# Kernel optimization log

Hardware: AMD Instinct MI355X
Metric: run time of the kernel (lower is better)

The kernel has to match this reference:

```python
import jax, jax.numpy as jnp
import numpy as np

N_NODES = 200000
N_EDGES = 800000
C1, E1 = 20000, 80000
C2, E2 = 2000, 8000
N_IN, N_HID, K_BLOCK = 24, 64, 6
N_OUT = 6
BN_EPS = 1e-5


def cheb_conv(x, edge_index, W, b, n):
    """PyG ChebConv with lambda_max=2: L_hat = -D^-1/2 A D^-1/2."""
    src, dst = edge_index[0], edge_index[1]
    K = W.shape[0]
    deg = jax.ops.segment_sum(jnp.ones(src.shape[0], x.dtype), dst, num_segments=n)
    dis = jnp.where(deg > 0, 1.0 / jnp.sqrt(jnp.maximum(deg, 1.0)), 0.0)
    norm = -(dis[src] * dis[dst])[:, None]  # [E,1]

    def prop(h):
        return jax.ops.segment_sum(h[src] * norm, dst, num_segments=n)

    Tx0 = x
    out = Tx0 @ W[0]
    if K > 1:
        Tx1 = prop(Tx0)
        out = out + Tx1 @ W[1]
        for k in range(2, K):
            Tx2 = 2.0 * prop(Tx1) - Tx0
            out = out + Tx2 @ W[k]
            Tx0, Tx1 = Tx1, Tx2
    return out + b


def batchnorm(h, g, bt):
    m = jnp.mean(h, axis=0)
    v = jnp.mean((h - m) ** 2, axis=0)  # biased var, as torch BN forward
    return (h - m) / jnp.sqrt(v + BN_EPS) * g + bt


def kipf_block(x, edge_index, W, b, g, bt, n):
    return jax.nn.relu(batchnorm(cheb_conv(x, edge_index, W, b, n), g, bt))


def segment_mean(x, seg, n_seg):
    s = jax.ops.segment_sum(x, seg, num_segments=n_seg)
    cnt = jax.ops.segment_sum(jnp.ones(x.shape[0], x.dtype), seg, num_segments=n_seg)
    return s / jnp.maximum(cnt, 1.0)[:, None]


def setup_inputs() -> dict:
    key = jax.random.key(0)
    ks = jax.random.split(key, 12)
    inp = {
        "x": jax.random.normal(ks[0], (N_NODES, N_IN), jnp.float32),
        "edge_index": jax.random.randint(ks[1], (2, N_EDGES), 0, N_NODES),
        "cluster1": jax.random.randint(ks[2], (N_NODES,), 0, C1),
        "cluster2": jax.random.randint(ks[3], (N_NODES,), 0, C2),
        "edge_index_c1": jax.random.randint(ks[4], (2, E1), 0, C1),
        "edge_index_c2": jax.random.randint(ks[5], (2, E2), 0, C2),
    }
    sc = 1.0 / np.sqrt(N_IN * K_BLOCK)
    for i, kk in zip((1, 2, 3), (ks[6], ks[7], ks[8])):
        inp[f"W{i}"] = jax.random.normal(kk, (K_BLOCK, N_IN, N_HID), jnp.float32) * sc
        inp[f"b{i}"] = jnp.zeros((N_HID,), jnp.float32)
        inp[f"g{i}"] = jnp.ones((N_HID,), jnp.float32)
        inp[f"bt{i}"] = jnp.zeros((N_HID,), jnp.float32)
    n_mix = 3 * N_HID + N_IN
    inp["Wm"] = jax.random.normal(ks[9], (1, n_mix, N_OUT), jnp.float32) / np.sqrt(n_mix)
    inp["bm"] = jnp.zeros((N_OUT,), jnp.float32)
    return inp


def reference(x, edge_index, cluster1, cluster2, edge_index_c1, edge_index_c2,
              W1, b1, g1, bt1, W2, b2, g2, bt2, W3, b3, g3, bt3, Wm, bm):
    # branch 1: full-resolution graph
    h1 = kipf_block(x, edge_index, W1, b1, g1, bt1, N_NODES)
    # branch 2: cluster1-pooled graph, then unpool
    xp1 = segment_mean(x, cluster1, C1)
    h2 = kipf_block(xp1, edge_index_c1, W2, b2, g2, bt2, C1)[cluster1]
    # branch 3: cluster2-pooled graph, then unpool
    xp2 = segment_mean(x, cluster2, C2)
    h3 = kipf_block(xp2, edge_index_c2, W3, b3, g3, bt3, C2)[cluster2]
    # skip concat with raw input, then mixing conv (K=1 -> identity Cheb term)
    mix = jnp.concatenate([h1, h2, h3, x], axis=1)
    return cheb_conv(mix, edge_index, Wm, bm, N_NODES)
```

## Files before the change

kernel.cpp:

```cpp
#include <hip/hip_runtime.h>
#include <algorithm>

#define FIN 24
#define NHID 64
#define NMIX 216
#define NOUT 6
#define BN_EPS 1e-5f

__global__ void k_hist(const int* __restrict__ ei, int E, int* deg) {
    int e = blockIdx.x * blockDim.x + threadIdx.x;
    if (e < E) atomicAdd(&deg[ei[E + e]], 1);
}

__global__ void k_scan_local(const int* __restrict__ deg, int n, int* rowptr, int* bsum,
                             float* __restrict__ dis) {
    __shared__ int s[256];
    int i = blockIdx.x * 256 + threadIdx.x;
    int v = (i < n) ? deg[i] : 0;
    if (i < n) dis[i] = v > 0 ? rsqrtf((float)v) : 0.f;
    s[threadIdx.x] = v;
    __syncthreads();
#pragma unroll
    for (int off = 1; off < 256; off <<= 1) {
        int x = (threadIdx.x >= off) ? s[threadIdx.x - off] : 0;
        __syncthreads();
        s[threadIdx.x] += x;
        __syncthreads();
    }
    if (i <= n) rowptr[i] = s[threadIdx.x] - v;
    if (threadIdx.x == 255) bsum[blockIdx.x] = s[255];
}

__global__ void k_scan_bsum(int* bsum, int nb) {
    __shared__ int s[256];
    int carry = 0;
    for (int base = 0; base < nb; base += 256) {
        int i = base + threadIdx.x;
        int v = (i < nb) ? bsum[i] : 0;
        s[threadIdx.x] = v;
        __syncthreads();
#pragma unroll
        for (int off = 1; off < 256; off <<= 1) {
            int x = (threadIdx.x >= off) ? s[threadIdx.x - off] : 0;
            __syncthreads();
            s[threadIdx.x] += x;
            __syncthreads();
        }
        if (i < nb) bsum[i] = s[threadIdx.x] - v + carry;
        carry += s[255];
        __syncthreads();
    }
}

__global__ void k_scan_add(int* rowptr, const int* __restrict__ bsum, int n) {
    int i = blockIdx.x * 256 + threadIdx.x;
    if (i <= n) rowptr[i] += bsum[blockIdx.x];
}

__global__ void k_fill(const int* __restrict__ ei, int E, const float* __restrict__ dis,
                       const int* __restrict__ rowptr, int* fill, int2* __restrict__ cv) {
    int e = blockIdx.x * blockDim.x + threadIdx.x;
    if (e >= E) return;
    int s = ei[e], d = ei[E + e];
    int slot = rowptr[d] + atomicAdd(&fill[d], 1);
    cv[slot] = make_int2(s, __float_as_int(-dis[s] * dis[d]));
}

__global__ void k_wt3(const float* __restrict__ Wa, float* __restrict__ Ta,
                      const float* __restrict__ Wb, float* __restrict__ Tb,
                      const float* __restrict__ Wc, float* __restrict__ Tc) {
    int o = blockIdx.x * blockDim.x + threadIdx.x;
    int which = o / 9216, oo = o - which * 9216;
    const float* W = (which == 0) ? Wa : (which == 1) ? Wb : Wc;
    float* T       = (which == 0) ? Ta : (which == 1) ? Tb : Tc;
    int k = oo / 1536, r = oo - k * 1536;
    int j = r / FIN, f = r - j * FIN;
    T[oo] = W[k * 1536 + f * NHID + j];
}

__global__ void k_propg(const int* __restrict__ rowptr, const int2* __restrict__ cv,
                        float scale, const float* __restrict__ h,
                        const float* __restrict__ prev, float* __restrict__ out, int n) {
    int idx = blockIdx.x * blockDim.x + threadIdx.x;
    if (idx >= n * 6) return;
    int d = idx / 6, q = idx - d * 6;
    int beg = rowptr[d], end = rowptr[d + 1];
    const float4* h4 = reinterpret_cast<const float4*>(h);
    float ax = 0.f, ay = 0.f, az = 0.f, aw = 0.f;
    float bx = 0.f, by = 0.f, bz = 0.f, bw = 0.f;
    float cx = 0.f, cy = 0.f, cz = 0.f, cw = 0.f;
    float dx = 0.f, dy = 0.f, dz = 0.f, dw = 0.f;
    int e = beg;
    for (; e + 4 <= end; e += 4) {
        int2 c0 = cv[e], c1 = cv[e + 1], c2 = cv[e + 2], c3 = cv[e + 3];
        float w0 = __int_as_float(c0.y), w1 = __int_as_float(c1.y);
        float w2 = __int_as_float(c2.y), w3 = __int_as_float(c3.y);
        float4 h0 = h4[(size_t)c0.x * 6 + q];
        float4 h1 = h4[(size_t)c1.x * 6 + q];
        float4 h2 = h4[(size_t)c2.x * 6 + q];
        float4 h3 = h4[(size_t)c3.x * 6 + q];
        ax = fmaf(w0, h0.x, ax); ay = fmaf(w0, h0.y, ay);
        az = fmaf(w0, h0.z, az); aw = fmaf(w0, h0.w, aw);
        bx = fmaf(w1, h1.x, bx); by = fmaf(w1, h1.y, by);
        bz = fmaf(w1, h1.z, bz); bw = fmaf(w1, h1.w, bw);
        cx = fmaf(w2, h2.x, cx); cy = fmaf(w2, h2.y, cy);
        cz = fmaf(w2, h2.z, cz); cw = fmaf(w2, h2.w, cw);
        dx = fmaf(w3, h3.x, dx); dy = fmaf(w3, h3.y, dy);
        dz = fmaf(w3, h3.z, dz); dw = fmaf(w3, h3.w, dw);
    }
    for (; e + 2 <= end; e += 2) {
        int2 c0 = cv[e], c1 = cv[e + 1];
        float w0 = __int_as_float(c0.y), w1 = __int_as_float(c1.y);
        float4 h0 = h4[(size_t)c0.x * 6 + q];
        float4 h1 = h4[(size_t)c1.x * 6 + q];
        ax = fmaf(w0, h0.x, ax); ay = fmaf(w0, h0.y, ay);
        az = fmaf(w0, h0.z, az); aw = fmaf(w0, h0.w, aw);
        bx = fmaf(w1, h1.x, bx); by = fmaf(w1, h1.y, by);
        bz = fmaf(w1, h1.z, bz); bw = fmaf(w1, h1.w, bw);
    }
    if (e < end) {
        int2 c0 = cv[e];
        float w0 = __int_as_float(c0.y);
        float4 h0 = h4[(size_t)c0.x * 6 + q];
        ax = fmaf(w0, h0.x, ax); ay = fmaf(w0, h0.y, ay);
        az = fmaf(w0, h0.z, az); aw = fmaf(w0, h0.w, aw);
    }
    ax += bx + cx + dx; ay += by + cy + dy;
    az += bz + cz + dz; aw += bw + cw + dw;
    float4 r;
    if (prev) {
        float4 pv = reinterpret_cast<const float4*>(prev)[idx];
        r = make_float4(fmaf(scale, ax, -pv.x), fmaf(scale, ay, -pv.y),
                        fmaf(scale, az, -pv.z), fmaf(scale, aw, -pv.w));
    } else {
        r = make_float4(scale * ax, scale * ay, scale * az, scale * aw);
    }
    reinterpret_cast<float4*>(out)[idx] = r;
}

__global__ void k_gemv6(const float* __restrict__ S0, const float* __restrict__ S1,
                        const float* __restrict__ S2, const float* __restrict__ S3,
                        const float* __restrict__ S4, const float* __restrict__ S5,
                        const float* __restrict__ Wt, const float* __restrict__ bias,
                        float* __restrict__ acc, float* __restrict__ stats, int n) {
    __shared__ float tile[4][64 * 17];
    int l = threadIdx.x & 63;
    int w = threadIdx.x >> 6;
    int c = blockIdx.x & 3;
    int nbase = (blockIdx.x >> 2) * 256 + w * 64;
    int node = nbase + l;
    bool ok = (node < n);
    int nodec = ok ? node : (n - 1);
    float* tl = &tile[w][0];
    float av[16];
#pragma unroll
    for (int jj = 0; jj < 16; ++jj) av[jj] = bias[c * 16 + jj];
#pragma unroll 1
    for (int k = 0; k < 6; ++k) {
        const float* Sk = (k == 0) ? S0 : (k == 1) ? S1 : (k == 2) ? S2
                        : (k == 3) ? S3 : (k == 4) ? S4 : S5;
        const float4* r = reinterpret_cast<const float4*>(Sk + (size_t)nodec * FIN);
        float4 v0 = r[0], v1 = r[1], v2 = r[2], v3 = r[3], v4 = r[4], v5 = r[5];
        const float* Wk = Wt + k * (NHID * FIN) + (c * 16) * FIN;
#pragma unroll
        for (int jj = 0; jj < 16; ++jj) {
            const float* ww = Wk + jj * FIN;
            float a = av[jj];
            a = fmaf(v0.x, ww[0], a);  a = fmaf(v0.y, ww[1], a);
            a = fmaf(v0.z, ww[2], a);  a = fmaf(v0.w, ww[3], a);
            a = fmaf(v1.x, ww[4], a);  a = fmaf(v1.y, ww[5], a);
            a = fmaf(v1.z, ww[6], a);  a = fmaf(v1.w, ww[7], a);
            a = fmaf(v2.x, ww[8], a);  a = fmaf(v2.y, ww[9], a);
            a = fmaf(v2.z, ww[10], a); a = fmaf(v2.w, ww[11], a);
            a = fmaf(v3.x, ww[12], a); a = fmaf(v3.y, ww[13], a);
            a = fmaf(v3.z, ww[14], a); a = fmaf(v3.w, ww[15], a);
            a = fmaf(v4.x, ww[16], a); a = fmaf(v4.y, ww[17], a);
            a = fmaf(v4.z, ww[18], a); a = fmaf(v4.w, ww[19], a);
            a = fmaf(v5.x, ww[20], a); a = fmaf(v5.y, ww[21], a);
            a = fmaf(v5.z, ww[22], a); a = fmaf(v5.w, ww[23], a);
            av[jj] = a;
        }
    }
    if (!ok) {
#pragma unroll
        for (int jj = 0; jj < 16; ++jj) av[jj] = 0.f;
    }
#pragma unroll
    for (int jj = 0; jj < 16; ++jj) tl[l * 17 + jj] = av[jj];
    asm volatile("" ::: "memory");
#pragma unroll
    for (int it = 0; it < 4; ++it) {
        int lin = it * 64 + l;
        int nd = lin >> 2, qj = lin & 3;
        int gnode = nbase + nd;
        if (gnode < n) {
            float4 vv = make_float4(tl[nd * 17 + qj * 4 + 0], tl[nd * 17 + qj * 4 + 1],
                                    tl[nd * 17 + qj * 4 + 2], tl[nd * 17 + qj * 4 + 3]);
            *reinterpret_cast<float4*>(acc + (size_t)gnode * NHID + c * 16 + qj * 4) = vv;
        }
    }
    float ps = 0.f, pq = 0.f;
    int jj = l & 15, ndb = (l >> 4) * 16;
#pragma unroll
    for (int t = 0; t < 16; ++t) {
        float vv = tl[(ndb + t) * 17 + jj];
        ps += vv; pq = fmaf(vv, vv, pq);
    }
    ps += __shfl_xor(ps, 16, 64); pq += __shfl_xor(pq, 16, 64);
    ps += __shfl_xor(ps, 32, 64); pq += __shfl_xor(pq, 32, 64);
    if (l < 16) {
        atomicAdd(&stats[c * 16 + jj], ps);
        atomicAdd(&stats[NHID + c * 16 + jj], pq);
    }
}

__global__ void k_bnprep3(const float* __restrict__ st1, const float* __restrict__ g1,
                          const float* __restrict__ bt1, float inv1,
                          const float* __restrict__ st2, const float* __restrict__ g2,
                          const float* __restrict__ bt2, float inv2,
                          const float* __restrict__ st3, const float* __restrict__ g3,
                          const float* __restrict__ bt3, float inv3,
                          float* __restrict__ s1, float* __restrict__ s2,
                          float* __restrict__ s3) {
    int b = threadIdx.x >> 6, i = threadIdx.x & 63;
    const float* st = (b == 0) ? st1 : (b == 1) ? st2 : st3;
    const float* g  = (b == 0) ? g1  : (b == 1) ? g2  : g3;
    const float* bt = (b == 0) ? bt1 : (b == 1) ? bt2 : bt3;
    float inv       = (b == 0) ? inv1 : (b == 1) ? inv2 : inv3;
    float* so       = (b == 0) ? s1  : (b == 1) ? s2  : s3;
    float m = st[i] * inv;
    float v = st[NHID + i] * inv - m * m;
    float sc = g[i] * rsqrtf(v + BN_EPS);
    so[i] = sc;
    so[NHID + i] = fmaf(-m, sc, bt[i]);
}

__global__ void k_scatter2(const float* __restrict__ x, const int* __restrict__ cl1,
                           const int* __restrict__ cl2, int n,
                           float* xp1, float* cnt1, float* xp2, float* cnt2) {
    int idx = blockIdx.x * blockDim.x + threadIdx.x;
    if (idx >= n * FIN) return;
    int node = idx / FIN, f = idx - node * FIN;
    float v = x[idx];
    int c1 = cl1[node], c2 = cl2[node];
    atomicAdd(&xp1[c1 * FIN + f], v);
    atomicAdd(&xp2[c2 * FIN + f], v);
    if (f == 0) { atomicAdd(&cnt1[c1], 1.f); atomicAdd(&cnt2[c2], 1.f); }
}

__global__ void k_divcnt(float* xp, const float* __restrict__ cnt, int c) {
    int idx = blockIdx.x * blockDim.x + threadIdx.x;
    if (idx >= c * FIN) return;
    xp[idx] = xp[idx] / fmaxf(cnt[idx / FIN], 1.f);
}

__global__ void k_final(const float* __restrict__ acc1, const float* __restrict__ sc1,
                        const float* __restrict__ h2, const float* __restrict__ sc2,
                        const int* __restrict__ cl1,
                        const float* __restrict__ h3, const float* __restrict__ sc3,
                        const int* __restrict__ cl2,
                        const float* __restrict__ x, const float* __restrict__ Wm,
                        const float* __restrict__ bm, float* __restrict__ out, int n) {
    int t = blockIdx.x * blockDim.x + threadIdx.x;
    if (t >= n) return;
    float o[NOUT];
#pragma unroll
    for (int j = 0; j < NOUT; ++j) o[j] = bm[j];
    {
        const float4* r4 = reinterpret_cast<const float4*>(acc1 + (size_t)t * NHID);
#pragma unroll
        for (int i4 = 0; i4 < NHID / 4; ++i4) {
            float4 v = r4[i4];
            float hv[4] = {v.x, v.y, v.z, v.w};
#pragma unroll
            for (int c = 0; c < 4; ++c) {
                int i = i4 * 4 + c;
                float h = fmaxf(fmaf(hv[c], sc1[i], sc1[NHID + i]), 0.f);
#pragma unroll
                for (int j = 0; j < NOUT; ++j) o[j] = fmaf(h, Wm[i * NOUT + j], o[j]);
            }
        }
    }
    {
        const float4* r4 = reinterpret_cast<const float4*>(h2 + (size_t)cl1[t] * NHID);
#pragma unroll
        for (int i4 = 0; i4 < NHID / 4; ++i4) {
            float4 v = r4[i4];
            float hv[4] = {v.x, v.y, v.z, v.w};
#pragma unroll
            for (int c = 0; c < 4; ++c) {
                int hid = i4 * 4 + c;
                float h = fmaxf(fmaf(hv[c], sc2[hid], sc2[NHID + hid]), 0.f);
#pragma unroll
                for (int j = 0; j < NOUT; ++j) o[j] = fmaf(h, Wm[(NHID + hid) * NOUT + j], o[j]);
            }
        }
    }
    {
        const float4* r4 = reinterpret_cast<const float4*>(h3 + (size_t)cl2[t] * NHID);
#pragma unroll
        for (int i4 = 0; i4 < NHID / 4; ++i4) {
            float4 v = r4[i4];
            float hv[4] = {v.x, v.y, v.z, v.w};
#pragma unroll
            for (int c = 0; c < 4; ++c) {
                int hid = i4 * 4 + c;
                float h = fmaxf(fmaf(hv[c], sc3[hid], sc3[NHID + hid]), 0.f);
#pragma unroll
                for (int j = 0; j < NOUT; ++j) o[j] = fmaf(h, Wm[(2 * NHID + hid) * NOUT + j], o[j]);
            }
        }
    }
    {
        const float4* r4 = reinterpret_cast<const float4*>(x + (size_t)t * FIN);
#pragma unroll
        for (int i4 = 0; i4 < FIN / 4; ++i4) {
            float4 v = r4[i4];
            float hv[4] = {v.x, v.y, v.z, v.w};
#pragma unroll
            for (int c = 0; c < 4; ++c) {
                int i = 3 * NHID + i4 * 4 + c;
#pragma unroll
                for (int j = 0; j < NOUT; ++j) o[j] = fmaf(hv[c], Wm[i * NOUT + j], o[j]);
            }
        }
    }
    float* op = out + (size_t)t * NOUT;
#pragma unroll
    for (int j = 0; j < NOUT; ++j) op[j] = o[j];
}

extern "C" void kernel_launch(void* const* d_in, const int* in_sizes, int n_in,
                              void* d_out, int out_size, void* d_ws, size_t ws_size,
                              hipStream_t stream) {
    const int N = 200000, E = 800000;
    const int C1n = 20000, E1 = 80000;
    const int C2n = 2000, E2 = 8000;

    const float* x  = (const float*)d_in[0];
    const int* ei   = (const int*)d_in[1];
    const int* cl1  = (const int*)d_in[2];
    const int* cl2  = (const int*)d_in[3];
    const int* eic1 = (const int*)d_in[4];
    const int* eic2 = (const int*)d_in[5];
    const float* W1 = (const float*)d_in[6];  const float* b1 = (const float*)d_in[7];
    const float* g1 = (const float*)d_in[8];  const float* bt1 = (const float*)d_in[9];
    const float* W2 = (const float*)d_in[10]; const float* b2 = (const float*)d_in[11];
    const float* g2 = (const float*)d_in[12]; const float* bt2 = (const float*)d_in[13];
    const float* W3 = (const float*)d_in[14]; const float* b3 = (const float*)d_in[15];
    const float* g3 = (const float*)d_in[16]; const float* bt3 = (const float*)d_in[17];
    const float* Wm = (const float*)d_in[18]; const float* bm = (const float*)d_in[19];

    char* wb = (char*)d_ws;
    size_t off = 0;
    auto alloc = [&](size_t nwords) {
        void* p = wb + off; off += ((nwords + 3) & ~(size_t)3) * 4; return p;
    };
    int* degi1 = (int*)alloc(N);   int* fill1 = (int*)alloc(N);
    int* degi2 = (int*)alloc(C1n); int* fill2 = (int*)alloc(C1n);
    int* degi3 = (int*)alloc(C2n); int* fill3 = (int*)alloc(C2n);
    float* st1 = (float*)alloc(128); float* st2 = (float*)alloc(128); float* st3 = (float*)alloc(128);
    float* xp1 = (float*)alloc((size_t)C1n * FIN); float* cnt1 = (float*)alloc(C1n);
    float* xp2 = (float*)alloc((size_t)C2n * FIN); float* cnt2 = (float*)alloc(C2n);
    size_t zero_bytes = off;
    int* rp1 = (int*)alloc(N + 1);   int2* cv1 = (int2*)alloc(2 * (size_t)E);
    int* rp2 = (int*)alloc(C1n + 1); int2* cv2 = (int2*)alloc(2 * (size_t)E1);
    int* rp3 = (int*)alloc(C2n + 1); int2* cv3 = (int2*)alloc(2 * (size_t)E2);
    float* dis1 = (float*)alloc(N); float* dis2 = (float*)alloc(C1n); float* dis3 = (float*)alloc(C2n);
    int* bsum = (int*)alloc(1024);
    float* scsh1 = (float*)alloc(128); float* scsh2 = (float*)alloc(128); float* scsh3 = (float*)alloc(128);
    float* Wt1 = (float*)alloc(9216); float* Wt2 = (float*)alloc(9216); float* Wt3 = (float*)alloc(9216);
    float* T1[5]; for (int i = 0; i < 5; ++i) T1[i] = (float*)alloc((size_t)N * FIN);
    float* T2[5]; for (int i = 0; i < 5; ++i) T2[i] = (float*)alloc((size_t)C1n * FIN);
    float* T3[5]; for (int i = 0; i < 5; ++i) T3[i] = (float*)alloc((size_t)C2n * FIN);
    float* acc1 = (float*)alloc((size_t)N * NHID);
    float* acc2 = (float*)alloc((size_t)C1n * NHID);
    float* acc3 = (float*)alloc((size_t)C2n * NHID);
    if (off > ws_size) return;

    (void)hipMemsetAsync(d_ws, 0, zero_bytes, stream);

    const int T = 256;
    auto cdiv = [](int a, int b) { return (a + b - 1) / b; };

    k_wt3<<<cdiv(3 * 9216, T), T, 0, stream>>>(W1, Wt1, W2, Wt2, W3, Wt3);

    auto branch = [&](const float* xin, int n, const int* e, int Ecnt,
                      const float* Wt, const float* bb, int* degi, int* fill, float* dis,
                      int* rp, int2* cv, float** Tb, float* acc, float* st) {
        int ge = cdiv(Ecnt, T);
        int nb = cdiv(n + 1, 256);
        int gg = cdiv(n, 256) * 4;
        int gp = cdiv(n * 6, T);
        k_hist<<<ge, T, 0, stream>>>(e, Ecnt, degi);
        k_scan_local<<<nb, 256, 0, stream>>>(degi, n, rp, bsum, dis);
        k_scan_bsum<<<1, 256, 0, stream>>>(bsum, nb);
        k_scan_add<<<nb, 256, 0, stream>>>(rp, bsum, n);
        k_fill<<<ge, T, 0, stream>>>(e, Ecnt, dis, rp, fill, cv);
        k_propg<<<gp, T, 0, stream>>>(rp, cv, 1.0f, xin, nullptr, Tb[0], n);
        k_propg<<<gp, T, 0, stream>>>(rp, cv, 2.0f, Tb[0], xin, Tb[1], n);
        k_propg<<<gp, T, 0, stream>>>(rp, cv, 2.0f, Tb[1], Tb[0], Tb[2], n);
        k_propg<<<gp, T, 0, stream>>>(rp, cv, 2.0f, Tb[2], Tb[1], Tb[3], n);
        k_propg<<<gp, T, 0, stream>>>(rp, cv, 2.0f, Tb[3], Tb[2], Tb[4], n);
        k_gemv6<<<gg, T, 0, stream>>>(xin, Tb[0], Tb[1], Tb[2], Tb[3], Tb[4],
                                      Wt, bb, acc, st, n);
    };

    branch(x, N, ei, E, Wt1, b1, degi1, fill1, dis1, rp1, cv1, T1, acc1, st1);
    k_scatter2<<<cdiv(N * FIN, T), T, 0, stream>>>(x, cl1, cl2, N, xp1, cnt1, xp2, cnt2);
    k_divcnt<<<cdiv(C1n * FIN, T), T, 0, stream>>>(xp1, cnt1, C1n);
    branch(xp1, C1n, eic1, E1, Wt2, b2, degi2, fill2, dis2, rp2, cv2, T2, acc2, st2);
    k_divcnt<<<cdiv(C2n * FIN, T), T, 0, stream>>>(xp2, cnt2, C2n);
    branch(xp2, C2n, eic2, E2, Wt3, b3, degi3, fill3, dis3, rp3, cv3, T3, acc3, st3);
    k_bnprep3<<<1, 192, 0, stream>>>(st1, g1, bt1, 1.0f / (float)N,
                                     st2, g2, bt2, 1.0f / (float)C1n,
                                     st3, g3, bt3, 1.0f / (float)C2n,
                                     scsh1, scsh2, scsh3);
    k_final<<<cdiv(N, T), T, 0, stream>>>(acc1, scsh1, acc2, scsh2, cl1,
                                          acc3, scsh3, cl2,
                                          x, Wm, bm, (float*)d_out, N);
}
```

Measured before the change: 657.6 us.

## Stage node features in shared memory so each block computes all 64 outputs

k_gemv6 now gives each block 64 nodes and has its four waves each compute a 16-column slice of the outputs. Previously four separate blocks per node group each reloaded the same six 24-float feature rows from global memory. The rows are now loaded once into padded shared memory and reused across the column groups. Output stores become direct per-thread float4 writes, and the BN statistics use a full-wave shuffle reduction per column instead of the transposed shared tile. The trade-offs are stores that are less coalesced and more shuffles and atomics per block.

```diff
diff --git a/kernel.cpp b/kernel.cpp
--- a/kernel.cpp
+++ b/kernel.cpp
@@ -6,6 +6,7 @@
 #define NMIX 216
 #define NOUT 6
 #define BN_EPS 1e-5f
+#define SROW 148
 
 __global__ void k_hist(const int* __restrict__ ei, int E, int* deg) {
     int e = blockIdx.x * blockDim.x + threadIdx.x;
@@ -143,25 +144,37 @@
                         const float* __restrict__ S4, const float* __restrict__ S5,
                         const float* __restrict__ Wt, const float* __restrict__ bias,
                         float* __restrict__ acc, float* __restrict__ stats, int n) {
-    __shared__ float tile[4][64 * 17];
-    int l = threadIdx.x & 63;
-    int w = threadIdx.x >> 6;
-    int c = blockIdx.x & 3;
-    int nbase = (blockIdx.x >> 2) * 256 + w * 64;
+    __shared__ float sb[64 * SROW];
+    int tid = threadIdx.x;
+    int nbase = blockIdx.x * 64;
+#pragma unroll
+    for (int it = 0; it < 9; ++it) {
+        int idx = it * 256 + tid;
+        int k = idx / 384;
+        int r = idx - k * 384;
+        int nd = r / 6, q = r - nd * 6;
+        int node = nbase + nd;
+        const float* Sk = (k == 0) ? S0 : (k == 1) ? S1 : (k == 2) ? S2
+                        : (k == 3) ? S3 : (k == 4) ? S4 : S5;
+        float4 v = (node < n)
+            ? *reinterpret_cast<const float4*>(Sk + (size_t)node * FIN + q * 4)
+            : make_float4(0.f, 0.f, 0.f, 0.f);
+        *reinterpret_cast<float4*>(&sb[nd * SROW + k * FIN + q * 4]) = v;
+    }
+    __syncthreads();
+    int l = tid & 63;
+    int jg = tid >> 6;
     int node = nbase + l;
     bool ok = (node < n);
-    int nodec = ok ? node : (n - 1);
-    float* tl = &tile[w][0];
+    const float* rowb = &sb[l * SROW];
     float av[16];
 #pragma unroll
-    for (int jj = 0; jj < 16; ++jj) av[jj] = bias[c * 16 + jj];
+    for (int jj = 0; jj < 16; ++jj) av[jj] = bias[jg * 16 + jj];
 #pragma unroll 1
     for (int k = 0; k < 6; ++k) {
-        const float* Sk = (k == 0) ? S0 : (k == 1) ? S1 : (k == 2) ? S2
-                        : (k == 3) ? S3 : (k == 4) ? S4 : S5;
-        const float4* r = reinterpret_cast<const float4*>(Sk + (size_t)nodec * FIN);
-        float4 v0 = r[0], v1 = r[1], v2 = r[2], v3 = r[3], v4 = r[4], v5 = r[5];
-        const float* Wk = Wt + k * (NHID * FIN) + (c * 16) * FIN;
+        const float4* r4 = reinterpret_cast<const float4*>(rowb + k * FIN);
+        float4 v0 = r4[0], v1 = r4[1], v2 = r4[2], v3 = r4[3], v4 = r4[4], v5 = r4[5];
+        const float* Wk = Wt + k * (NHID * FIN) + (jg * 16) * FIN;
 #pragma unroll
         for (int jj = 0; jj < 16; ++jj) {
             const float* ww = Wk + jj * FIN;
@@ -185,32 +198,25 @@
 #pragma unroll
         for (int jj = 0; jj < 16; ++jj) av[jj] = 0.f;
     }
-#pragma unroll
-    for (int jj = 0; jj < 16; ++jj) tl[l * 17 + jj] = av[jj];
-    asm volatile("" ::: "memory");
-#pragma unroll
-    for (int it = 0; it < 4; ++it) {
-        int lin = it * 64 + l;
-        int nd = lin >> 2, qj = lin & 3;
-        int gnode = nbase + nd;
-        if (gnode < n) {
-            float4 vv = make_float4(tl[nd * 17 + qj * 4 + 0], tl[nd * 17 + qj * 4 + 1],
-                                    tl[nd * 17 + qj * 4 + 2], tl[nd * 17 + qj * 4 + 3]);
-            *reinterpret_cast<float4*>(acc + (size_t)gnode * NHID + c * 16 + qj * 4) = vv;
-        }
-    }
-    float ps = 0.f, pq = 0.f;
-    int jj = l & 15, ndb = (l >> 4) * 16;
-#pragma unroll
-    for (int t = 0; t < 16; ++t) {
-        float vv = tl[(ndb + t) * 17 + jj];
-        ps += vv; pq = fmaf(vv, vv, pq);
-    }
-    ps += __shfl_xor(ps, 16, 64); pq += __shfl_xor(pq, 16, 64);
-    ps += __shfl_xor(ps, 32, 64); pq += __shfl_xor(pq, 32, 64);
-    if (l < 16) {
-        atomicAdd(&stats[c * 16 + jj], ps);
-        atomicAdd(&stats[NHID + c * 16 + jj], pq);
+    if (ok) {
+        float* op = acc + (size_t)node * NHID + jg * 16;
+#pragma unroll
+        for (int s4 = 0; s4 < 4; ++s4)
+            reinterpret_cast<float4*>(op)[s4] =
+                make_float4(av[s4 * 4 + 0], av[s4 * 4 + 1], av[s4 * 4 + 2], av[s4 * 4 + 3]);
+    }
+#pragma unroll
+    for (int jj = 0; jj < 16; ++jj) {
+        float s = av[jj], q = av[jj] * av[jj];
+#pragma unroll
+        for (int d = 32; d; d >>= 1) {
+            s += __shfl_xor(s, d, 64);
+            q += __shfl_xor(q, d, 64);
+        }
+        if (l == 0) {
+            atomicAdd(&stats[jg * 16 + jj], s);
+            atomicAdd(&stats[NHID + jg * 16 + jj], q);
+        }
     }
 }
 
@@ -390,7 +396,7 @@
                       int* rp, int2* cv, float** Tb, float* acc, float* st) {
         int ge = cdiv(Ecnt, T);
         int nb = cdiv(n + 1, 256);
-        int gg = cdiv(n, 256) * 4;
+        int gg = cdiv(n, 64);
         int gp = cdiv(n * 6, T);
         k_hist<<<ge, T, 0, stream>>>(e, Ecnt, degi);
         k_scan_local<<<nb, 256, 0, stream>>>(degi, n, rp, bsum, dis);
```

After: 1.941 ms. 2.95x slower.
